# Kernel tuning notes

Measured on AMD Instinct MI355X. Metric: run time of the kernel, lower is better.

The kernel has to match this reference:

```python
import jax, jax.numpy as jnp
import numpy as np

FEAT_DIM = 16
NUM_DEPTHS = 64


def _lookat(p):
    z = p / np.linalg.norm(p)
    up = np.array([0.0, 1.0, 0.0])
    x = np.cross(up, z); x = x / np.linalg.norm(x)
    y = np.cross(z, x)
    m = np.eye(4)
    m[:3, 0] = x; m[:3, 1] = y; m[:3, 2] = z; m[:3, 3] = p
    return m


def setup_inputs() -> dict:
    key = jax.random.key(0)
    ks = jax.random.split(key, 6)
    S, Vin, Vt, C, D, H, W = 2, 3, 4, FEAT_DIM, NUM_DEPTHS, 96, 96
    enc = jax.random.normal(ks[0], (S, Vin, C, D, H, W), jnp.float32) * 0.5
    rng = np.random.default_rng(0)

    def poses(n):
        ps = rng.normal(size=(S, n, 3))
        ps = ps / np.linalg.norm(ps, axis=-1, keepdims=True) * 1.3
        return jnp.asarray(np.stack([[_lookat(ps[i, j]) for j in range(n)] for i in range(S)]), jnp.float32)

    input_poses = poses(Vin)
    target_poses = poses(Vt)
    W1 = jax.random.normal(ks[1], (16, 64), jnp.float32) * 0.25
    W2 = jax.random.normal(ks[2], (64, 64), jnp.float32) * 0.125
    W3 = jax.random.normal(ks[3], (64, 17), jnp.float32) * 0.125
    return dict(
        encoded_imgs=enc, input_poses=input_poses, target_poses=target_poses,
        focal=1.2, z_near=0.8, z_far=1.8, samples_per_ray=64,
        W1=W1, b1=jnp.zeros((64,), jnp.float32),
        W2=W2, b2=jnp.zeros((64,), jnp.float32),
        W3=W3, b3=jnp.zeros((17,), jnp.float32),
    )


def grid_sample_3d(vol, grid):
    # vol: (N,C,D,H,W); grid: (N,P,3) xyz in [-1,1]; trilinear, zero padding, align_corners=False
    N, C, D, H, W = vol.shape
    P = grid.shape[1]
    ix = ((grid[..., 0] + 1.0) * W - 1.0) * 0.5
    iy = ((grid[..., 1] + 1.0) * H - 1.0) * 0.5
    iz = ((grid[..., 2] + 1.0) * D - 1.0) * 0.5
    x0, y0, z0 = jnp.floor(ix), jnp.floor(iy), jnp.floor(iz)
    volf = vol.reshape(N, C, D * H * W)
    out = jnp.zeros((N, C, P), vol.dtype)
    for dz in (0, 1):
        for dy in (0, 1):
            for dx in (0, 1):
                xc, yc, zc = x0 + dx, y0 + dy, z0 + dz
                wgt = (1.0 - jnp.abs(ix - xc)) * (1.0 - jnp.abs(iy - yc)) * (1.0 - jnp.abs(iz - zc))
                valid = ((xc >= 0) & (xc < W) & (yc >= 0) & (yc < H) & (zc >= 0) & (zc < D))
                xi = jnp.clip(xc, 0, W - 1).astype(jnp.int32)
                yi = jnp.clip(yc, 0, H - 1).astype(jnp.int32)
                zi = jnp.clip(zc, 0, D - 1).astype(jnp.int32)
                idx = (zi * H + yi) * W + xi  # (N,P)
                vals = jnp.take_along_axis(volf, idx[:, None, :], axis=2)  # (N,C,P)
                out = out + (wgt * valid)[:, None, :] * vals
    return out


def _upsample2_align_corners(x):
    # bilinear x2 on last two axes, align_corners=True (torch UpsamplingBilinear2d)
    def interp(x, axis):
        n = x.shape[axis]
        m = 2 * n
        pos = jnp.arange(m) * ((n - 1) / (m - 1))
        lo = jnp.floor(pos).astype(jnp.int32)
        hi = jnp.minimum(lo + 1, n - 1)
        f = (pos - lo).astype(x.dtype)
        xl = jnp.take(x, lo, axis=axis)
        xh = jnp.take(x, hi, axis=axis)
        shp = [1] * x.ndim; shp[axis] = m
        f = f.reshape(shp)
        return xl * (1.0 - f) + xh * f
    return interp(interp(x, -2), -1)


def _forward(encoded_imgs, input_poses, target_poses, focal, z_near, z_far,
             samples_per_ray, W1, b1, W2, b2, W3, b3):
    S, Vin, C, D, H, W = encoded_imgs.shape
    Vt = target_poses.shape[1]
    h, w = H // 2, W // 2
    spr = samples_per_ray
    dt = encoded_imgs.dtype

    # --- gen_rays at half resolution ---
    poses = target_poses.reshape(S * Vt, 4, 4)
    ys = ((jnp.arange(h, dtype=dt) + 0.5) / h) * 2.0 - 1.0
    xs = ((jnp.arange(w, dtype=dt) + 0.5) / w) * 2.0 - 1.0
    yy, xx = jnp.meshgrid(ys, xs, indexing='ij')
    dirs_cam = jnp.stack([xx / focal, -yy / focal, -jnp.ones_like(xx)], -1)  # (h,w,3)
    dirs = jnp.einsum('bij,hwj->bhwi', poses[:, :3, :3], dirs_cam)            # (B,h,w,3)
    origins = poses[:, None, None, :3, 3]                                      # (B,1,1,3)

    t = z_near + (z_far - z_near) * (jnp.arange(spr, dtype=dt) / (spr - 1))
    times = jnp.broadcast_to(t, (S * Vt, h, w, spr))
    pts = origins[..., None, :] + times[..., None] * dirs[..., None, :]        # (B,h,w,spr,3)

    times = times.reshape(S, Vt, h, w, spr)
    pts = pts.reshape(S, Vt, h, w, spr, 3)
    pts_h = jnp.concatenate([pts, jnp.ones_like(pts[..., :1])], axis=-1)      # (S,Vt,h,w,spr,4)

    # --- invert input poses (rigid) ---
    R = input_poses[..., :3, :3]
    tr = input_poses[..., :3, 3]
    Rt = jnp.swapaxes(R, -1, -2)
    inv_t = -jnp.einsum('svij,svj->svi', Rt, tr)
    top = jnp.concatenate([Rt, inv_t[..., None]], axis=-1)                     # (S,Vin,3,4)
    bottom = jnp.broadcast_to(jnp.array([0.0, 0.0, 0.0, 1.0], dt), (S, Vin, 1, 4))
    extrinsics = jnp.concatenate([top, bottom], axis=-2)                       # (S,Vin,4,4)

    local = jnp.einsum('svij,sthwpj->svthwpi', extrinsics, pts_h)              # (S,Vin,Vt,h,w,spr,4)
    x = local[..., 0]
    y = local[..., 1]
    z = -local[..., 2]
    u = x / z * focal
    v = y / z * focal
    min_z, max_z = focal * z_near, focal * z_far
    wd = 2.0 * (z - min_z) / (max_z - min_z) - 1.0
    uvw = jnp.stack((u, -v, -wd), axis=-1)                                     # (S,Vin,Vt,h,w,spr,3)

    feats = grid_sample_3d(encoded_imgs.reshape(S * Vin, C, D, H, W),
                           uvw.reshape(S * Vin, -1, 3))                        # (S*Vin,C,P)
    feats = feats.reshape(S, Vin, C, Vt, h, w, spr)
    feats = jnp.mean(feats, axis=1)                                            # baseline_mean camera weighting
    feats = jnp.transpose(feats, (0, 2, 3, 4, 5, 1))                           # (S,Vt,h,w,spr,C)

    # --- MLP with residual feature skip ---
    x1 = jax.nn.relu(feats @ W1 + b1)
    x2 = jax.nn.relu(x1 @ W2 + b2)
    out = x2 @ W3 + b3                                                         # (...,17)
    density = jax.nn.relu(out[..., 0])
    rgb = feats + out[..., 1:]

    # --- volume rendering ---
    deltas = times[..., 1:] - times[..., :-1]
    last = jnp.full_like(deltas[..., :1], 1e10)
    deltas = jnp.concatenate([deltas, last], axis=-1)
    sigdel = density * deltas
    alpha = 1.0 - jnp.exp(-sigdel)
    transmittance = jnp.exp(-jnp.cumsum(sigdel, axis=-1))
    wts = alpha * transmittance
    renders = jnp.sum(wts[..., None] * rgb, axis=-2)                           # (S,Vt,h,w,16)

    renders = jnp.transpose(renders, (0, 1, 4, 2, 3))                          # (S,Vt,16,h,w)
    renders = _upsample2_align_corners(renders.reshape(S * Vt, C, h, w))
    return renders.reshape(S, Vt, C, H, W)


def reference(encoded_imgs, input_poses, target_poses, focal, z_near, z_far,
              samples_per_ray, W1, b1, W2, b2, W3, b3):
    return _forward(encoded_imgs, input_poses, target_poses, float(focal), float(z_near),
                    float(z_far), int(samples_per_ray), W1, b1, W2, b2, W3, b3)
```

## Files before the change

kernel.cpp:

```cpp
#include <hip/hip_runtime.h>
#include <hip/hip_bf16.h>
#include <math.h>

#define NS   2
#define NVIN 3
#define NVT  4
#define NC   16
#define ND   64
#define NH   96
#define NW   96
#define HWH  48
#define SPR  64
#define DHW  (ND*NH*NW)
#define NTILE (DHW / 64)

typedef __attribute__((ext_vector_type(8))) short bfrag;
typedef __attribute__((ext_vector_type(4))) float cfrag;

#define MFMA16 __builtin_amdgcn_mfma_f32_16x16x32_bf16

__device__ __forceinline__ short f2bf(float x) {
    union { __hip_bfloat16 b; short s; } cv;
    cv.b = __float2bfloat16(x);
    return cv.s;
}
__device__ __forceinline__ float bf2f(short s) {
    union { unsigned int u; float f; } cv;
    cv.u = ((unsigned int)(unsigned short)s) << 16;
    return cv.f;
}

__device__ __forceinline__ void mk_frag(const float* p, bfrag& ah, bfrag& al) {
    float4 v0 = *(const float4*)p;
    float4 v1 = *(const float4*)(p + 4);
    float e[8] = {v0.x, v0.y, v0.z, v0.w, v1.x, v1.y, v1.z, v1.w};
    #pragma unroll
    for (int j = 0; j < 8; j++) {
        short h = f2bf(e[j]);
        ah[j] = h;
        al[j] = f2bf(e[j] - bf2f(h));
    }
}

__global__ __launch_bounds__(256) void wprep_kernel(
    const float* __restrict__ W1, const float* __restrict__ W2,
    const float* __restrict__ W3, short* __restrict__ whi, short* __restrict__ wlo)
{
    int t = blockIdx.x * 256 + threadIdx.x;
    int f = t >> 6, L = t & 63;
    int q = L >> 4, li = L & 15;
    #pragma unroll
    for (int j = 0; j < 8; j++) {
        int kloc = q * 8 + j;
        float w = 0.f;
        if (f < 4) {
            int n = f * 16 + li, k = kloc;
            if (k < 16) w = W1[k * 64 + n];
        } else if (f < 12) {
            int kt = (f - 4) >> 2, nt = (f - 4) & 3;
            w = W2[(kt * 32 + kloc) * 64 + nt * 16 + li];
        } else {
            int kt = (f - 12) >> 1, nt = (f - 12) & 1;
            int n = nt * 16 + li;
            if (n < 17) w = W3[(kt * 32 + kloc) * 17 + n];
        }
        short h = f2bf(w);
        whi[(f * 64 + L) * 8 + j] = h;
        wlo[(f * 64 + L) * 8 + j] = f2bf(w - bf2f(h));
    }
}

__global__ __launch_bounds__(256) void transpose_kernel(
    const float* __restrict__ in, float* __restrict__ out)
{
    __shared__ float tile[NC][64 + 4];
    const int t   = threadIdx.x;
    const int blk = blockIdx.x;
    const int vox0 = (blk % NTILE) * 64;
    const int sv   = blk / NTILE;

    const int c  = t >> 4;
    const int vg = (t & 15) * 4;
    const float* src = in + ((size_t)sv * NC + c) * DHW + vox0 + vg;
    float4 v = *(const float4*)src;
    tile[c][vg + 0] = v.x; tile[c][vg + 1] = v.y;
    tile[c][vg + 2] = v.z; tile[c][vg + 3] = v.w;
    __syncthreads();

    const int ov = t >> 2;
    const int oc = (t & 3) * 4;
    float4 w = make_float4(tile[oc + 0][ov], tile[oc + 1][ov],
                           tile[oc + 2][ov], tile[oc + 3][ov]);
    float* dst = out + ((size_t)sv * DHW + vox0 + ov) * NC + oc;
    *(float4*)dst = w;
}

__global__ __launch_bounds__(256) void render_mfma_kernel(
    const float* __restrict__ enc_t,
    const float* __restrict__ ipose,
    const float* __restrict__ tpose,
    const float* __restrict__ focal_p,
    const float* __restrict__ znear_p,
    const float* __restrict__ zfar_p,
    const short* __restrict__ whi, const short* __restrict__ wlo,
    const float* __restrict__ B1, const float* __restrict__ B2,
    const float* __restrict__ B3,
    float* __restrict__ rhalf)
{
    const int lane = threadIdx.x & 63;
    const int ray  = blockIdx.x * 4 + (threadIdx.x >> 6);
    const int px   = ray % HWH;
    const int py   = (ray / HWH) % HWH;
    const int b    = ray / (HWH * HWH);
    const int s    = b >> 2;

    const float focal = focal_p[0];
    const float znear = znear_p[0];
    const float zfar  = zfar_p[0];

    const float* P = tpose + b * 16;
    float ysc = ((py + 0.5f) / (float)HWH) * 2.f - 1.f;
    float xsc = ((px + 0.5f) / (float)HWH) * 2.f - 1.f;
    float dcx = xsc / focal, dcy = -ysc / focal, dcz = -1.f;
    float dirx = P[0]*dcx + P[1]*dcy + P[2]*dcz;
    float diry = P[4]*dcx + P[5]*dcy + P[6]*dcz;
    float dirz = P[8]*dcx + P[9]*dcy + P[10]*dcz;
    float ox = P[3], oy = P[7], oz = P[11];

    float tv  = znear + (zfar - znear) * ((float)lane / (float)(SPR - 1));
    float ptx = ox + tv * dirx, pty = oy + tv * diry, ptz = oz + tv * dirz;

    float feats[NC];
    #pragma unroll
    for (int c = 0; c < NC; c++) feats[c] = 0.f;

    const float minz = focal * znear, maxz = focal * zfar;

    for (int v = 0; v < NVIN; v++) {
        const float* E = ipose + (s * NVIN + v) * 16;
        float qx = ptx - E[3], qy = pty - E[7], qz = ptz - E[11];
        float lx = E[0]*qx + E[4]*qy + E[8]*qz;
        float ly = E[1]*qx + E[5]*qy + E[9]*qz;
        float lz = E[2]*qx + E[6]*qy + E[10]*qz;
        float zz = -lz;
        float u  = lx / zz * focal;
        float vv = ly / zz * focal;
        float wd = 2.f * (zz - minz) / (maxz - minz) - 1.f;
        float ix = ((u   + 1.f) * NW - 1.f) * 0.5f;
        float iy = ((-vv + 1.f) * NH - 1.f) * 0.5f;
        float iz = ((-wd + 1.f) * ND - 1.f) * 0.5f;
        float x0 = floorf(ix), y0 = floorf(iy), z0 = floorf(iz);

        float wgt[8]; int idx[8];
        #pragma unroll
        for (int k = 0; k < 8; k++) {
            float xc = x0 + (k & 1), yc = y0 + ((k >> 1) & 1), zc = z0 + (k >> 2);
            float wt = (1.f - fabsf(ix - xc)) * (1.f - fabsf(iy - yc)) * (1.f - fabsf(iz - zc));
            bool valid = (xc >= 0.f) && (xc < (float)NW) &&
                         (yc >= 0.f) && (yc < (float)NH) &&
                         (zc >= 0.f) && (zc < (float)ND);
            wgt[k] = valid ? wt : 0.f;
            int xi = min(max((int)xc, 0), NW - 1);
            int yi = min(max((int)yc, 0), NH - 1);
            int zi = min(max((int)zc, 0), ND - 1);
            idx[k] = (zi * NH + yi) * NW + xi;
        }
        const float* VB = enc_t + (size_t)(s * NVIN + v) * DHW * NC;
        #pragma unroll
        for (int k = 0; k < 8; k++) {
            const float* p = VB + (size_t)idx[k] * NC;
            float4 a0 = *(const float4*)(p);
            float4 a1 = *(const float4*)(p + 4);
            float4 a2 = *(const float4*)(p + 8);
            float4 a3 = *(const float4*)(p + 12);
            float w = wgt[k];
            feats[0]  += w * a0.x; feats[1]  += w * a0.y;
            feats[2]  += w * a0.z; feats[3]  += w * a0.w;
            feats[4]  += w * a1.x; feats[5]  += w * a1.y;
            feats[6]  += w * a1.z; feats[7]  += w * a1.w;
            feats[8]  += w * a2.x; feats[9]  += w * a2.y;
            feats[10] += w * a2.z; feats[11] += w * a2.w;
            feats[12] += w * a3.x; feats[13] += w * a3.y;
            feats[14] += w * a3.z; feats[15] += w * a3.w;
        }
    }
    #pragma unroll
    for (int c = 0; c < NC; c++) feats[c] *= (1.f / 3.f);

    __shared__ float sbuf[4][64][36];
    float (*B)[36] = sbuf[threadIdx.x >> 6];
    const int li = lane & 15, q = lane >> 4;

    float b1v[4], b2v[4], b3v[2];
    #pragma unroll
    for (int nt = 0; nt < 4; nt++) { b1v[nt] = B1[nt*16 + li]; b2v[nt] = B2[nt*16 + li]; }
    b3v[0] = B3[li];
    b3v[1] = (li == 0) ? B3[16] : 0.f;

    *(float4*)&B[lane][0]  = make_float4(feats[0], feats[1], feats[2],  feats[3]);
    *(float4*)&B[lane][4]  = make_float4(feats[4], feats[5], feats[6],  feats[7]);
    *(float4*)&B[lane][8]  = make_float4(feats[8], feats[9], feats[10], feats[11]);
    *(float4*)&B[lane][12] = make_float4(feats[12], feats[13], feats[14], feats[15]);
    float4 z4 = make_float4(0.f, 0.f, 0.f, 0.f);
    *(float4*)&B[lane][16] = z4; *(float4*)&B[lane][20] = z4;
    *(float4*)&B[lane][24] = z4; *(float4*)&B[lane][28] = z4;
    __syncthreads();

    bfrag xah[4], xal[4];
    #pragma unroll
    for (int mt = 0; mt < 4; mt++)
        mk_frag(&B[mt*16 + li][q*8], xah[mt], xal[mt]);

    cfrag zc = {0.f, 0.f, 0.f, 0.f};
    cfrag h2acc[4][4];
    #pragma unroll
    for (int mt = 0; mt < 4; mt++)
        #pragma unroll
        for (int nt = 0; nt < 4; nt++) h2acc[mt][nt] = zc;

    #pragma unroll
    for (int c1 = 0; c1 < 2; c1++) {
        cfrag h1[4][2];
        #pragma unroll
        for (int nt2 = 0; nt2 < 2; nt2++) {
            int f = 2*c1 + nt2;
            bfrag bh = *(const bfrag*)(whi + (f*64 + lane)*8);
            bfrag bl = *(const bfrag*)(wlo + (f*64 + lane)*8);
            #pragma unroll
            for (int mt = 0; mt < 4; mt++) {
                cfrag a = zc;
                a = MFMA16(xal[mt], bh, a, 0, 0, 0);
                a = MFMA16(xah[mt], bl, a, 0, 0, 0);
                a = MFMA16(xah[mt], bh, a, 0, 0, 0);
                h1[mt][nt2] = a;
            }
        }
        __syncthreads();
        #pragma unroll
        for (int mt = 0; mt < 4; mt++)
            #pragma unroll
            for (int nt2 = 0; nt2 < 2; nt2++)
                #pragma unroll
                for (int r = 0; r < 4; r++)
                    B[mt*16 + q*4 + r][nt2*16 + li] =
                        fmaxf(h1[mt][nt2][r] + b1v[2*c1 + nt2], 0.f);
        __syncthreads();
        bfrag hah[4], hal[4];
        #pragma unroll
        for (int mt = 0; mt < 4; mt++)
            mk_frag(&B[mt*16 + li][q*8], hah[mt], hal[mt]);
        #pragma unroll
        for (int nt = 0; nt < 4; nt++) {
            int f = 4 + c1*4 + nt;
            bfrag bh = *(const bfrag*)(whi + (f*64 + lane)*8);
            bfrag bl = *(const bfrag*)(wlo + (f*64 + lane)*8);
            #pragma unroll
            for (int mt = 0; mt < 4; mt++) {
                cfrag a = h2acc[mt][nt];
                a = MFMA16(hal[mt], bh, a, 0, 0, 0);
                a = MFMA16(hah[mt], bl, a, 0, 0, 0);
                a = MFMA16(hah[mt], bh, a, 0, 0, 0);
                h2acc[mt][nt] = a;
            }
        }
    }

    cfrag oacc[4][2];
    #pragma unroll
    for (int mt = 0; mt < 4; mt++)
        #pragma unroll
        for (int nt = 0; nt < 2; nt++) oacc[mt][nt] = zc;

    #pragma unroll
    for (int c2 = 0; c2 < 2; c2++) {
        __syncthreads();
        #pragma unroll
        for (int mt = 0; mt < 4; mt++)
            #pragma unroll
            for (int nt2 = 0; nt2 < 2; nt2++)
                #pragma unroll
                for (int r = 0; r < 4; r++)
                    B[mt*16 + q*4 + r][nt2*16 + li] =
                        fmaxf(h2acc[mt][2*c2 + nt2][r] + b2v[2*c2 + nt2], 0.f);
        __syncthreads();
        bfrag hah[4], hal[4];
        #pragma unroll
        for (int mt = 0; mt < 4; mt++)
            mk_frag(&B[mt*16 + li][q*8], hah[mt], hal[mt]);
        #pragma unroll
        for (int nt = 0; nt < 2; nt++) {
            int f = 12 + c2*2 + nt;
            bfrag bh = *(const bfrag*)(whi + (f*64 + lane)*8);
            bfrag bl = *(const bfrag*)(wlo + (f*64 + lane)*8);
            #pragma unroll
            for (int mt = 0; mt < 4; mt++) {
                cfrag a = oacc[mt][nt];
                a = MFMA16(hal[mt], bh, a, 0, 0, 0);
                a = MFMA16(hah[mt], bl, a, 0, 0, 0);
                a = MFMA16(hah[mt], bh, a, 0, 0, 0);
                oacc[mt][nt] = a;
            }
        }
    }

    __syncthreads();
    #pragma unroll
    for (int mt = 0; mt < 4; mt++)
        #pragma unroll
        for (int nt = 0; nt < 2; nt++) {
            int ch = nt*16 + li;
            if (ch < 17) {
                #pragma unroll
                for (int r = 0; r < 4; r++)
                    B[mt*16 + q*4 + r][ch] = oacc[mt][nt][r] + b3v[nt];
            }
        }
    __syncthreads();
    float4 o0 = *(float4*)&B[lane][0];
    float4 o1 = *(float4*)&B[lane][4];
    float4 o2 = *(float4*)&B[lane][8];
    float4 o3 = *(float4*)&B[lane][12];
    float o16 = B[lane][16];

    float density = fmaxf(o0.x, 0.f);
    float orgb[16] = {o0.y, o0.z, o0.w, o1.x, o1.y, o1.z, o1.w, o2.x,
                      o2.y, o2.z, o2.w, o3.x, o3.y, o3.z, o3.w, o16};

    float tn = znear + (zfar - znear) * ((float)(lane + 1) / (float)(SPR - 1));
    float delta = (lane < SPR - 1) ? (tn - tv) : 1e10f;
    float sigdel = density * delta;
    float alpha = 1.f - expf(-sigdel);
    float csum = sigdel;
    #pragma unroll
    for (int off = 1; off < 64; off <<= 1) {
        float nb = __shfl_up(csum, off, 64);
        if (lane >= off) csum += nb;
    }
    float wray = alpha * expf(-csum);

    #pragma unroll
    for (int c = 0; c < NC; c++) {
        float val = wray * (feats[c] + orgb[c]);
        #pragma unroll
        for (int off = 32; off >= 1; off >>= 1)
            val += __shfl_down(val, off, 64);
        if (lane == 0)
            rhalf[((b * NC + c) * HWH + py) * HWH + px] = val;
    }
}

__device__ __forceinline__ void mlp_and_composite(
    const float feats[NC], int lane, int b, int py, int px,
    float tv, float znear, float zfar,
    const float* __restrict__ W1, const float* __restrict__ B1,
    const float* __restrict__ W2, const float* __restrict__ B2,
    const float* __restrict__ W3, const float* __restrict__ B3,
    float* __restrict__ rhalf)
{
    float outa[17];
    #pragma unroll
    for (int c = 0; c < 17; c++) outa[c] = B3[c];

    for (int kc = 0; kc < 4; kc++) {
        float h2c[16];
        #pragma unroll
        for (int k = 0; k < 16; k++) h2c[k] = B2[kc * 16 + k];
        #pragma unroll 4
        for (int j = 0; j < 64; j++) {
            float a = B1[j];
            #pragma unroll
            for (int i = 0; i < NC; i++) a += feats[i] * W1[i * 64 + j];
            a = fmaxf(a, 0.f);
            const float* w2p = W2 + j * 64 + kc * 16;
            #pragma unroll
            for (int k = 0; k < 16; k++) h2c[k] += a * w2p[k];
        }
        #pragma unroll
        for (int k = 0; k < 16; k++) {
            float hv = fmaxf(h2c[k], 0.f);
            const float* w3p = W3 + (kc * 16 + k) * 17;
            #pragma unroll
            for (int c = 0; c < 17; c++) outa[c] += hv * w3p[c];
        }
    }
    float density = fmaxf(outa[0], 0.f);

    float tn = znear + (zfar - znear) * ((float)(lane + 1) / (float)(SPR - 1));
    float delta = (lane < SPR - 1) ? (tn - tv) : 1e10f;
    float sigdel = density * delta;
    float alpha = 1.f - expf(-sigdel);
    float csum = sigdel;
    #pragma unroll
    for (int off = 1; off < 64; off <<= 1) {
        float nb = __shfl_up(csum, off, 64);
        if (lane >= off) csum += nb;
    }
    float wray = alpha * expf(-csum);

    #pragma unroll
    for (int c = 0; c < NC; c++) {
        float val = wray * (feats[c] + outa[1 + c]);
        #pragma unroll
        for (int off = 32; off >= 1; off >>= 1)
            val += __shfl_down(val, off, 64);
        if (lane == 0)
            rhalf[((b * NC + c) * HWH + py) * HWH + px] = val;
    }
}

__global__ __launch_bounds__(256) void render_kernel(
    const float* __restrict__ enc,
    const float* __restrict__ ipose,
    const float* __restrict__ tpose,
    const float* __restrict__ focal_p,
    const float* __restrict__ znear_p,
    const float* __restrict__ zfar_p,
    const float* __restrict__ W1, const float* __restrict__ B1,
    const float* __restrict__ W2, const float* __restrict__ B2,
    const float* __restrict__ W3, const float* __restrict__ B3,
    float* __restrict__ rhalf)
{
    const int lane = threadIdx.x & 63;
    const int ray  = blockIdx.x * 4 + (threadIdx.x >> 6);
    const int px   = ray % HWH;
    const int py   = (ray / HWH) % HWH;
    const int b    = ray / (HWH * HWH);
    const int s    = b >> 2;

    const float focal = focal_p[0];
    const float znear = znear_p[0];
    const float zfar  = zfar_p[0];

    const float* P = tpose + b * 16;
    float ysc = ((py + 0.5f) / (float)HWH) * 2.f - 1.f;
    float xsc = ((px + 0.5f) / (float)HWH) * 2.f - 1.f;
    float dcx = xsc / focal, dcy = -ysc / focal, dcz = -1.f;
    float dirx = P[0]*dcx + P[1]*dcy + P[2]*dcz;
    float diry = P[4]*dcx + P[5]*dcy + P[6]*dcz;
    float dirz = P[8]*dcx + P[9]*dcy + P[10]*dcz;
    float ox = P[3], oy = P[7], oz = P[11];

    float tv  = znear + (zfar - znear) * ((float)lane / (float)(SPR - 1));
    float ptx = ox + tv * dirx, pty = oy + tv * diry, ptz = oz + tv * dirz;

    float feats[NC];
    #pragma unroll
    for (int c = 0; c < NC; c++) feats[c] = 0.f;

    const float minz = focal * znear, maxz = focal * zfar;

    for (int v = 0; v < NVIN; v++) {
        const float* E = ipose + (s * NVIN + v) * 16;
        float qx = ptx - E[3], qy = pty - E[7], qz = ptz - E[11];
        float lx = E[0]*qx + E[4]*qy + E[8]*qz;
        float ly = E[1]*qx + E[5]*qy + E[9]*qz;
        float lz = E[2]*qx + E[6]*qy + E[10]*qz;
        float zz = -lz;
        float u  = lx / zz * focal;
        float vv = ly / zz * focal;
        float wd = 2.f * (zz - minz) / (maxz - minz) - 1.f;
        float ix = ((u   + 1.f) * NW - 1.f) * 0.5f;
        float iy = ((-vv + 1.f) * NH - 1.f) * 0.5f;
        float iz = ((-wd + 1.f) * ND - 1.f) * 0.5f;
        float x0 = floorf(ix), y0 = floorf(iy), z0 = floorf(iz);

        float wgt[8]; int idx[8];
        #pragma unroll
        for (int k = 0; k < 8; k++) {
            float xc = x0 + (k & 1), yc = y0 + ((k >> 1) & 1), zc = z0 + (k >> 2);
            float wt = (1.f - fabsf(ix - xc)) * (1.f - fabsf(iy - yc)) * (1.f - fabsf(iz - zc));
            bool valid = (xc >= 0.f) && (xc < (float)NW) &&
                         (yc >= 0.f) && (yc < (float)NH) &&
                         (zc >= 0.f) && (zc < (float)ND);
            wgt[k] = valid ? wt : 0.f;
            int xi = min(max((int)xc, 0), NW - 1);
            int yi = min(max((int)yc, 0), NH - 1);
            int zi = min(max((int)zc, 0), ND - 1);
            idx[k] = (zi * NH + yi) * NW + xi;
        }
        const float* VB = enc + (size_t)(s * NVIN + v) * NC * DHW;
        #pragma unroll
        for (int c = 0; c < NC; c++) {
            const float* vc = VB + c * DHW;
            float acc = 0.f;
            #pragma unroll
            for (int k = 0; k < 8; k++) acc += wgt[k] * vc[idx[k]];
            feats[c] += acc;
        }
    }
    #pragma unroll
    for (int c = 0; c < NC; c++) feats[c] *= (1.f / 3.f);

    mlp_and_composite(feats, lane, b, py, px, tv, znear, zfar,
                      W1, B1, W2, B2, W3, B3, rhalf);
}

__global__ __launch_bounds__(256) void upsample_kernel(
    const float* __restrict__ in, float* __restrict__ out)
{
    int tid = blockIdx.x * 256 + threadIdx.x;
    int ox = tid % NW;
    int oy = (tid / NW) % NH;
    int c  = (tid / (NW * NH)) % NC;
    int b  = tid / (NW * NH * NC);
    const float sc = (float)((HWH - 1) / (double)(NH - 1));
    float pyf = oy * sc;
    float pxf = ox * sc;
    int y0 = (int)floorf(pyf); int y1 = min(y0 + 1, HWH - 1); float fy = pyf - y0;
    int x0 = (int)floorf(pxf); int x1 = min(x0 + 1, HWH - 1); float fx = pxf - x0;
    const float* src = in + (b * NC + c) * HWH * HWH;
    float v00 = src[y0 * HWH + x0], v01 = src[y0 * HWH + x1];
    float v10 = src[y1 * HWH + x0], v11 = src[y1 * HWH + x1];
    float gl = v00 * (1.f - fy) + v10 * fy;
    float gr = v01 * (1.f - fy) + v11 * fy;
    out[tid] = gl * (1.f - fx) + gr * fx;
}

extern "C" void kernel_launch(void* const* d_in, const int* in_sizes, int n_in,
                              void* d_out, int out_size, void* d_ws, size_t ws_size,
                              hipStream_t stream) {
    const float* enc   = (const float*)d_in[0];
    const float* ipose = (const float*)d_in[1];
    const float* tpose = (const float*)d_in[2];
    const float* focal = (const float*)d_in[3];
    const float* znear = (const float*)d_in[4];
    const float* zfar  = (const float*)d_in[5];
    const float* W1 = (const float*)d_in[7];
    const float* B1 = (const float*)d_in[8];
    const float* W2 = (const float*)d_in[9];
    const float* B2 = (const float*)d_in[10];
    const float* W3 = (const float*)d_in[11];
    const float* B3 = (const float*)d_in[12];

    float* out = (float*)d_out;
    const int nrays = NS * NVT * HWH * HWH;
    const int nout  = NS * NVT * NC * NH * NW;
    const size_t enc_t_bytes = (size_t)NS * NVIN * NC * DHW * 4;
    const size_t rhalf_bytes = (size_t)NS * NVT * NC * HWH * HWH * 4;
    const size_t wfrag_bytes = 16 * 64 * 8 * sizeof(short);

    if (ws_size >= enc_t_bytes + rhalf_bytes + 2 * wfrag_bytes) {
        float* enc_t = (float*)d_ws;
        float* rhalf = (float*)((char*)d_ws + enc_t_bytes);
        short* whi   = (short*)((char*)d_ws + enc_t_bytes + rhalf_bytes);
        short* wlo   = whi + 16 * 64 * 8;

        wprep_kernel<<<4, 256, 0, stream>>>(W1, W2, W3, whi, wlo);
        const int ntiles = NS * NVIN * NTILE;
        transpose_kernel<<<ntiles, 256, 0, stream>>>(enc, enc_t);
        render_mfma_kernel<<<nrays / 4, 256, 0, stream>>>(
            enc_t, ipose, tpose, focal, znear, zfar,
            whi, wlo, B1, B2, B3, rhalf);
        upsample_kernel<<<nout / 256, 256, 0, stream>>>(rhalf, out);
    } else {
        float* rhalf = (float*)d_ws;
        render_kernel<<<nrays / 4, 256, 0, stream>>>(
            enc, ipose, tpose, focal, znear, zfar,
            W1, B1, W2, B2, W3, B3, rhalf);
        upsample_kernel<<<nout / 256, 256, 0, stream>>>(rhalf, out);
    }
}
```

Before: 727.1 us.

## Split fused render kernel into separate gather and MLP kernels via workspace buffer

The fused render kernel is split into a gather kernel and an MLP kernel. The gather kernel assigns four threads per sample, one per float4 channel group, for trilinear sampling and writes the averaged features to a global buffer. The MLP kernel then reads those features directly into MFMA fragments and does the compositing. This raises memory-level parallelism in the gather and lowers register pressure, but adds a global write and re-read of the features (about 75 MB) plus an extra launch.

```diff
diff --git a/kernel.cpp b/kernel.cpp
--- a/kernel.cpp
+++ b/kernel.cpp
@@ -13,6 +13,7 @@
 #define SPR  64
 #define DHW  (ND*NH*NW)
 #define NTILE (DHW / 64)
+#define NSAMP (NS*NVT*HWH*HWH*SPR)
 
 typedef __attribute__((ext_vector_type(8))) short bfrag;
 typedef __attribute__((ext_vector_type(4))) float cfrag;
@@ -95,24 +96,24 @@
     *(float4*)dst = w;
 }
 
-__global__ __launch_bounds__(256) void render_mfma_kernel(
+__global__ __launch_bounds__(256) void gather_kernel(
     const float* __restrict__ enc_t,
     const float* __restrict__ ipose,
     const float* __restrict__ tpose,
     const float* __restrict__ focal_p,
     const float* __restrict__ znear_p,
     const float* __restrict__ zfar_p,
-    const short* __restrict__ whi, const short* __restrict__ wlo,
-    const float* __restrict__ B1, const float* __restrict__ B2,
-    const float* __restrict__ B3,
-    float* __restrict__ rhalf)
-{
-    const int lane = threadIdx.x & 63;
-    const int ray  = blockIdx.x * 4 + (threadIdx.x >> 6);
-    const int px   = ray % HWH;
-    const int py   = (ray / HWH) % HWH;
-    const int b    = ray / (HWH * HWH);
-    const int s    = b >> 2;
+    float* __restrict__ xbuf)
+{
+    const int tid = blockIdx.x * 256 + threadIdx.x;
+    const int c4  = tid & 3;
+    const int smp = tid >> 2;
+    const int d   = smp & 63;
+    const int ray = smp >> 6;
+    const int px  = ray % HWH;
+    const int py  = (ray / HWH) % HWH;
+    const int b   = ray / (HWH * HWH);
+    const int s   = b >> 2;
 
     const float focal = focal_p[0];
     const float znear = znear_p[0];
@@ -125,16 +126,12 @@
     float dirx = P[0]*dcx + P[1]*dcy + P[2]*dcz;
     float diry = P[4]*dcx + P[5]*dcy + P[6]*dcz;
     float dirz = P[8]*dcx + P[9]*dcy + P[10]*dcz;
-    float ox = P[3], oy = P[7], oz = P[11];
-
-    float tv  = znear + (zfar - znear) * ((float)lane / (float)(SPR - 1));
-    float ptx = ox + tv * dirx, pty = oy + tv * diry, ptz = oz + tv * dirz;
-
-    float feats[NC];
-    #pragma unroll
-    for (int c = 0; c < NC; c++) feats[c] = 0.f;
+
+    float tv  = znear + (zfar - znear) * ((float)d / (float)(SPR - 1));
+    float ptx = P[3] + tv * dirx, pty = P[7] + tv * diry, ptz = P[11] + tv * dirz;
 
     const float minz = focal * znear, maxz = focal * zfar;
+    float f0 = 0.f, f1 = 0.f, f2 = 0.f, f3 = 0.f;
 
     for (int v = 0; v < NVIN; v++) {
         const float* E = ipose + (s * NVIN + v) * 16;
@@ -151,7 +148,7 @@
         float iz = ((-wd + 1.f) * ND - 1.f) * 0.5f;
         float x0 = floorf(ix), y0 = floorf(iy), z0 = floorf(iz);
 
-        float wgt[8]; int idx[8];
+        const float* VB = enc_t + (size_t)(s * NVIN + v) * DHW * NC;
         #pragma unroll
         for (int k = 0; k < 8; k++) {
             float xc = x0 + (k & 1), yc = y0 + ((k >> 1) & 1), zc = z0 + (k >> 2);
@@ -159,37 +156,41 @@
             bool valid = (xc >= 0.f) && (xc < (float)NW) &&
                          (yc >= 0.f) && (yc < (float)NH) &&
                          (zc >= 0.f) && (zc < (float)ND);
-            wgt[k] = valid ? wt : 0.f;
+            float w = valid ? wt : 0.f;
             int xi = min(max((int)xc, 0), NW - 1);
             int yi = min(max((int)yc, 0), NH - 1);
             int zi = min(max((int)zc, 0), ND - 1);
-            idx[k] = (zi * NH + yi) * NW + xi;
-        }
-        const float* VB = enc_t + (size_t)(s * NVIN + v) * DHW * NC;
-        #pragma unroll
-        for (int k = 0; k < 8; k++) {
-            const float* p = VB + (size_t)idx[k] * NC;
-            float4 a0 = *(const float4*)(p);
-            float4 a1 = *(const float4*)(p + 4);
-            float4 a2 = *(const float4*)(p + 8);
-            float4 a3 = *(const float4*)(p + 12);
-            float w = wgt[k];
-            feats[0]  += w * a0.x; feats[1]  += w * a0.y;
-            feats[2]  += w * a0.z; feats[3]  += w * a0.w;
-            feats[4]  += w * a1.x; feats[5]  += w * a1.y;
-            feats[6]  += w * a1.z; feats[7]  += w * a1.w;
-            feats[8]  += w * a2.x; feats[9]  += w * a2.y;
-            feats[10] += w * a2.z; feats[11] += w * a2.w;
-            feats[12] += w * a3.x; feats[13] += w * a3.y;
-            feats[14] += w * a3.z; feats[15] += w * a3.w;
-        }
-    }
-    #pragma unroll
-    for (int c = 0; c < NC; c++) feats[c] *= (1.f / 3.f);
+            int idx = (zi * NH + yi) * NW + xi;
+            float4 a = *(const float4*)(VB + (size_t)idx * NC + c4 * 4);
+            f0 += w * a.x; f1 += w * a.y; f2 += w * a.z; f3 += w * a.w;
+        }
+    }
+    const float inv3 = 1.f / 3.f;
+    ((float4*)xbuf)[tid] = make_float4(f0 * inv3, f1 * inv3, f2 * inv3, f3 * inv3);
+}
+
+__global__ __launch_bounds__(256) void mlp_kernel(
+    const float* __restrict__ xbuf,
+    const float* __restrict__ znear_p,
+    const float* __restrict__ zfar_p,
+    const short* __restrict__ whi, const short* __restrict__ wlo,
+    const float* __restrict__ B1, const float* __restrict__ B2,
+    const float* __restrict__ B3,
+    float* __restrict__ rhalf)
+{
+    const int lane = threadIdx.x & 63;
+    const int ray  = blockIdx.x * 4 + (threadIdx.x >> 6);
+    const int px   = ray % HWH;
+    const int py   = (ray / HWH) % HWH;
+    const int b    = ray / (HWH * HWH);
+
+    const float znear = znear_p[0];
+    const float zfar  = zfar_p[0];
 
     __shared__ float sbuf[4][64][36];
     float (*B)[36] = sbuf[threadIdx.x >> 6];
     const int li = lane & 15, q = lane >> 4;
+    const float* X = xbuf + (size_t)ray * 64 * NC;
 
     float b1v[4], b2v[4], b3v[2];
     #pragma unroll
@@ -197,19 +198,13 @@
     b3v[0] = B3[li];
     b3v[1] = (li == 0) ? B3[16] : 0.f;
 
-    *(float4*)&B[lane][0]  = make_float4(feats[0], feats[1], feats[2],  feats[3]);
-    *(float4*)&B[lane][4]  = make_float4(feats[4], feats[5], feats[6],  feats[7]);
-    *(float4*)&B[lane][8]  = make_float4(feats[8], feats[9], feats[10], feats[11]);
-    *(float4*)&B[lane][12] = make_float4(feats[12], feats[13], feats[14], feats[15]);
-    float4 z4 = make_float4(0.f, 0.f, 0.f, 0.f);
-    *(float4*)&B[lane][16] = z4; *(float4*)&B[lane][20] = z4;
-    *(float4*)&B[lane][24] = z4; *(float4*)&B[lane][28] = z4;
-    __syncthreads();
-
     bfrag xah[4], xal[4];
-    #pragma unroll
-    for (int mt = 0; mt < 4; mt++)
-        mk_frag(&B[mt*16 + li][q*8], xah[mt], xal[mt]);
+    bfrag zb = {0,0,0,0,0,0,0,0};
+    #pragma unroll
+    for (int mt = 0; mt < 4; mt++) {
+        if (q < 2) mk_frag(X + (mt*16 + li) * NC + q * 8, xah[mt], xal[mt]);
+        else { xah[mt] = zb; xal[mt] = zb; }
+    }
 
     cfrag zc = {0.f, 0.f, 0.f, 0.f};
     cfrag h2acc[4][4];
@@ -326,6 +321,14 @@
     float orgb[16] = {o0.y, o0.z, o0.w, o1.x, o1.y, o1.z, o1.w, o2.x,
                       o2.y, o2.z, o2.w, o3.x, o3.y, o3.z, o3.w, o16};
 
+    float4 fx0 = *(const float4*)(X + lane * NC + 0);
+    float4 fx1 = *(const float4*)(X + lane * NC + 4);
+    float4 fx2 = *(const float4*)(X + lane * NC + 8);
+    float4 fx3 = *(const float4*)(X + lane * NC + 12);
+    float feats[16] = {fx0.x, fx0.y, fx0.z, fx0.w, fx1.x, fx1.y, fx1.z, fx1.w,
+                       fx2.x, fx2.y, fx2.z, fx2.w, fx3.x, fx3.y, fx3.z, fx3.w};
+
+    float tv = znear + (zfar - znear) * ((float)lane / (float)(SPR - 1));
     float tn = znear + (zfar - znear) * ((float)(lane + 1) / (float)(SPR - 1));
     float delta = (lane < SPR - 1) ? (tn - tv) : 1e10f;
     float sigdel = density * delta;
@@ -360,7 +363,6 @@
     float outa[17];
     #pragma unroll
     for (int c = 0; c < 17; c++) outa[c] = B3[c];
-
     for (int kc = 0; kc < 4; kc++) {
         float h2c[16];
         #pragma unroll
@@ -384,7 +386,6 @@
         }
     }
     float density = fmaxf(outa[0], 0.f);
-
     float tn = znear + (zfar - znear) * ((float)(lane + 1) / (float)(SPR - 1));
     float delta = (lane < SPR - 1) ? (tn - tv) : 1e10f;
     float sigdel = density * delta;
@@ -396,7 +397,6 @@
         if (lane >= off) csum += nb;
     }
     float wray = alpha * expf(-csum);
-
     #pragma unroll
     for (int c = 0; c < NC; c++) {
         float val = wray * (feats[c] + outa[1 + c]);
@@ -426,11 +426,9 @@
     const int py   = (ray / HWH) % HWH;
     const int b    = ray / (HWH * HWH);
     const int s    = b >> 2;
-
     const float focal = focal_p[0];
     const float znear = znear_p[0];
     const float zfar  = zfar_p[0];
-
     const float* P = tpose + b * 16;
     float ysc = ((py + 0.5f) / (float)HWH) * 2.f - 1.f;
     float xsc = ((px + 0.5f) / (float)HWH) * 2.f - 1.f;
@@ -438,17 +436,12 @@
     float dirx = P[0]*dcx + P[1]*dcy + P[2]*dcz;
     float diry = P[4]*dcx + P[5]*dcy + P[6]*dcz;
     float dirz = P[8]*dcx + P[9]*dcy + P[10]*dcz;
-    float ox = P[3], oy = P[7], oz = P[11];
-
     float tv  = znear + (zfar - znear) * ((float)lane / (float)(SPR - 1));
-    float ptx = ox + tv * dirx, pty = oy + tv * diry, ptz = oz + tv * dirz;
-
+    float ptx = P[3] + tv * dirx, pty = P[7] + tv * diry, ptz = P[11] + tv * dirz;
     float feats[NC];
     #pragma unroll
     for (int c = 0; c < NC; c++) feats[c] = 0.f;
-
     const float minz = focal * znear, maxz = focal * zfar;
-
     for (int v = 0; v < NVIN; v++) {
         const float* E = ipose + (s * NVIN + v) * 16;
         float qx = ptx - E[3], qy = pty - E[7], qz = ptz - E[11];
@@ -463,7 +456,6 @@
         float iy = ((-vv + 1.f) * NH - 1.f) * 0.5f;
         float iz = ((-wd + 1.f) * ND - 1.f) * 0.5f;
         float x0 = floorf(ix), y0 = floorf(iy), z0 = floorf(iz);
-
         float wgt[8]; int idx[8];
         #pragma unroll
         for (int k = 0; k < 8; k++) {
@@ -490,7 +482,6 @@
     }
     #pragma unroll
     for (int c = 0; c < NC; c++) feats[c] *= (1.f / 3.f);
-
     mlp_and_composite(feats, lane, b, py, px, tv, znear, zfar,
                       W1, B1, W2, B2, W3, B3, rhalf);
 }
@@ -536,21 +527,24 @@
     const int nrays = NS * NVT * HWH * HWH;
     const int nout  = NS * NVT * NC * NH * NW;
     const size_t enc_t_bytes = (size_t)NS * NVIN * NC * DHW * 4;
-    const size_t rhalf_bytes = (size_t)NS * NVT * NC * HWH * HWH * 4;
+    const size_t rhalf_bytes = (size_t)nrays * NC * 4;
     const size_t wfrag_bytes = 16 * 64 * 8 * sizeof(short);
-
-    if (ws_size >= enc_t_bytes + rhalf_bytes + 2 * wfrag_bytes) {
-        float* enc_t = (float*)d_ws;
-        float* rhalf = (float*)((char*)d_ws + enc_t_bytes);
-        short* whi   = (short*)((char*)d_ws + enc_t_bytes + rhalf_bytes);
-        short* wlo   = whi + 16 * 64 * 8;
+    const size_t xbuf_bytes  = (size_t)NSAMP * NC * 4;
+
+    if (ws_size >= enc_t_bytes + rhalf_bytes + 2 * wfrag_bytes + xbuf_bytes) {
+        char* base = (char*)d_ws;
+        float* enc_t = (float*)base;                      base += enc_t_bytes;
+        float* rhalf = (float*)base;                      base += rhalf_bytes;
+        short* whi   = (short*)base;                      base += wfrag_bytes;
+        short* wlo   = (short*)base;                      base += wfrag_bytes;
+        float* xbuf  = (float*)base;
 
         wprep_kernel<<<4, 256, 0, stream>>>(W1, W2, W3, whi, wlo);
-        const int ntiles = NS * NVIN * NTILE;
-        transpose_kernel<<<ntiles, 256, 0, stream>>>(enc, enc_t);
-        render_mfma_kernel<<<nrays / 4, 256, 0, stream>>>(
-            enc_t, ipose, tpose, focal, znear, zfar,
-            whi, wlo, B1, B2, B3, rhalf);
+        transpose_kernel<<<NS * NVIN * NTILE, 256, 0, stream>>>(enc, enc_t);
+        gather_kernel<<<NSAMP * 4 / 256, 256, 0, stream>>>(
+            enc_t, ipose, tpose, focal, znear, zfar, xbuf);
+        mlp_kernel<<<nrays / 4, 256, 0, stream>>>(
+            xbuf, znear, zfar, whi, wlo, B1, B2, B3, rhalf);
         upsample_kernel<<<nout / 256, 256, 0, stream>>>(rhalf, out);
     } else {
         float* rhalf = (float*)d_ws;
```

Result: faster. 616.9 us (-15.2%).
